# Kernel tuning notes

Measured on AMD Instinct MI355X. Metric: run time of the kernel, lower is better.

## Reference

```python
import jax, jax.numpy as jnp
import numpy as np

D = 1024
LD = 64
NTR = 8192
NT = 8192
DY = 128

def setup_inputs() -> dict:
    key = jax.random.key(0)
    k1, k2, k3, k4 = jax.random.split(key, 4)
    xtr = jax.random.normal(k1, (NTR, D), dtype=jnp.float32)
    ytr = jax.random.normal(k2, (NTR, DY), dtype=jnp.float32)
    xt = jax.random.normal(k3, (NT, D), dtype=jnp.float32)
    A = jax.random.normal(k4, (D, LD), dtype=jnp.float32) / (D ** 0.5)
    return {"xtr": xtr, "ytr": ytr, "xt": xt, "A": A}

def reference(xtr, ytr, xt, A):
    # mean-center both train and test features with the train mean
    mu = jnp.mean(xtr, axis=0, keepdims=True)          # [1, d]
    qtr = (xtr - mu) @ A                                # [Ntr, ld]
    qt = (xt - mu) @ A                                  # [Nt, ld]
    scores = jnp.einsum('nl,ml->nm', qt, qtr)           # [Nt, Ntr]
    E = jax.nn.softmax(scores, axis=1)                  # row-wise softmax over train points
    return E @ ytr                                      # [Nt, dy]
```

## Files before the change

kernel.cpp:

```cpp
#include <hip/hip_runtime.h>
#include <hip/hip_bf16.h>

#define D    1024
#define LD   64
#define NTR  8192
#define NT   8192
#define DY   128

#define SHIFT 40.0f
#define NCHUNK 8
#define CHUNK (NTR / NCHUNK)

typedef __attribute__((ext_vector_type(8))) short bf16x8;
typedef __attribute__((ext_vector_type(8))) _Float16 half8;
typedef __attribute__((ext_vector_type(4))) short short4_;
typedef __attribute__((ext_vector_type(4))) float f4;

static __device__ __forceinline__ short f2bf(float f) {
    __hip_bfloat16 h = __float2bfloat16(f);
    short s; __builtin_memcpy(&s, &h, 2); return s;
}
static __device__ __forceinline__ float bf2f(short s) {
    __hip_bfloat16 h; __builtin_memcpy(&h, &s, 2); return __bfloat162float(h);
}
static __device__ __forceinline__ short f2h(float f) {
    _Float16 h = (_Float16)f;
    short s; __builtin_memcpy(&s, &h, 2); return s;
}
static __device__ __forceinline__ float h2f(short s) {
    _Float16 h; __builtin_memcpy(&h, &s, 2); return (float)h;
}

static __device__ __forceinline__ void gload_lds16(const void* g, void* l) {
    __builtin_amdgcn_global_load_lds(
        (const __attribute__((address_space(1))) unsigned int*)g,
        (__attribute__((address_space(3))) unsigned int*)l,
        16, 0, 0);
}

__global__ __launch_bounds__(256) void proj_prep(const float* __restrict__ xt,
                                                 const float* __restrict__ xtr,
                                                 const float* __restrict__ A,
                                                 const float* __restrict__ ytr,
                                                 short* __restrict__ qt_hi,
                                                 short* __restrict__ qt_lo,
                                                 short* __restrict__ ktr,
                                                 float* __restrict__ muAp,
                                                 short* __restrict__ vtile) {
    __shared__ __align__(16) float smem[4224];

    int tid = threadIdx.x;
    int b = blockIdx.x;

    if (b >= 1024) {
        float* tile = smem;
        int bz = b - 1024;
        int t0 = (bz & 127) * 64;
        int d0 = (bz >> 7) * 64;
        int c = tid & 63;
        int r4 = tid >> 6;
        #pragma unroll
        for (int i = 0; i < 16; ++i) {
            int r = i * 4 + r4;
            tile[r * 66 + c] = ytr[(long)(t0 + r) * DY + d0 + c];
        }
        __syncthreads();
        #pragma unroll
        for (int i = 0; i < 16; ++i) {
            int r = i * 4 + r4;
            int t = t0 + c;
            int dy = d0 + r;
            long idx = (long)(t >> 5) * 4096 + (long)dy * 32
                     + ((((t >> 3) & 3) ^ (dy & 3)) << 3) + (t & 7);
            vtile[idx] = f2bf(tile[c * 66 + r]);
        }
        return;
    }

    float (*xbuf)[2][1024] = (float (*)[2][1024])smem;

    int wave = tid >> 6;
    int lane = tid & 63;
    int quad = lane >> 4;
    int l16 = lane & 15;

    bool is_test = b < (NT / 16);
    int row0 = (is_test ? b : b - NT / 16) * 16;
    const float* x = is_test ? xt : xtr;

    int lr = wave * 4 + (lane >> 4);
    int cg = (lane & 15) ^ (lr & 7);
    const float* xsrc = x + (long)(row0 + lr) * D + cg * 4;

    int col = wave * 16 + l16;
    const float* Acol = A + col;

    f4 acc = (f4){0.f, 0.f, 0.f, 0.f};

    int pr0 = ((quad * 2) ^ (l16 & 7)) * 4;
    int pr1 = (((quad * 2) | 1) ^ (l16 & 7)) * 4;

    gload_lds16(xsrc, &xbuf[0][0][wave * 256]);
    gload_lds16(xsrc + 64, &xbuf[0][1][wave * 256]);
    __syncthreads();

    #pragma unroll 1
    for (int s = 0; s < 8; ++s) {
        int cur = s & 1;
        if (s < 7) {
            const float* nsrc = xsrc + (s + 1) * 128;
            gload_lds16(nsrc, &xbuf[cur ^ 1][0][wave * 256]);
            gload_lds16(nsrc + 64, &xbuf[cur ^ 1][1][wave * 256]);
        }

        #pragma unroll
        for (int s2 = 0; s2 < 2; ++s2) {
            int k0 = s * 128 + s2 * 64;

            bf16x8 bh0, bh1, bl0, bl1;
            #pragma unroll
            for (int j = 0; j < 8; ++j) {
                float a0 = Acol[(long)(k0 + quad * 8 + j) * LD];
                float a1 = Acol[(long)(k0 + 32 + quad * 8 + j) * LD];
                short h0 = f2bf(a0);
                short h1 = f2bf(a1);
                bh0[j] = h0; bl0[j] = f2bf(a0 - bf2f(h0));
                bh1[j] = h1; bl1[j] = f2bf(a1 - bf2f(h1));
            }

            const float* xrow = &xbuf[cur][s2][l16 * 64];
            bf16x8 ah[2], al[2];
            #pragma unroll
            for (int h = 0; h < 2; ++h) {
                f4 v0 = *(const f4*)(xrow + h * 32 + pr0);
                f4 v1 = *(const f4*)(xrow + h * 32 + pr1);
                #pragma unroll
                for (int e = 0; e < 4; ++e) {
                    short hi0 = f2bf(v0[e]);
                    short hi1 = f2bf(v1[e]);
                    ah[h][e]     = hi0;
                    ah[h][e + 4] = hi1;
                    al[h][e]     = f2bf(v0[e] - bf2f(hi0));
                    al[h][e + 4] = f2bf(v1[e] - bf2f(hi1));
                }
            }
            acc = __builtin_amdgcn_mfma_f32_16x16x32_bf16(ah[0], bh0, acc, 0, 0, 0);
            acc = __builtin_amdgcn_mfma_f32_16x16x32_bf16(al[0], bh0, acc, 0, 0, 0);
            acc = __builtin_amdgcn_mfma_f32_16x16x32_bf16(ah[0], bl0, acc, 0, 0, 0);
            acc = __builtin_amdgcn_mfma_f32_16x16x32_bf16(ah[1], bh1, acc, 0, 0, 0);
            acc = __builtin_amdgcn_mfma_f32_16x16x32_bf16(al[1], bh1, acc, 0, 0, 0);
            acc = __builtin_amdgcn_mfma_f32_16x16x32_bf16(ah[1], bl1, acc, 0, 0, 0);
        }
        __syncthreads();
    }

    #pragma unroll
    for (int r = 0; r < 4; ++r) {
        int grow = row0 + quad * 4 + r;
        float qv = acc[r];
        if (is_test) {
            short hi = f2h(qv);
            qt_hi[(long)grow * LD + col] = hi;
            qt_lo[(long)grow * LD + col] = f2h(qv - h2f(hi));
        } else {
            int tl = grow & 31;
            long idx = (long)(grow >> 5) * 2048 + tl * 64
                     + ((((col >> 3) ^ (tl & 7))) << 3) + (col & 7);
            ktr[idx] = f2h(qv);
        }
    }

    if (!is_test) {
        float s = acc[0] + acc[1] + acc[2] + acc[3];
        s += __shfl_xor(s, 16);
        s += __shfl_xor(s, 32);
        if (quad == 0) muAp[(long)(b - NT / 16) * 64 + col] = s;
    }
}

__global__ __launch_bounds__(256) void c_kernel(const short* __restrict__ ktr,
                                                const float* __restrict__ muAp,
                                                float* __restrict__ cc) {
    __shared__ float red[4][64];
    __shared__ __align__(16) float muAs[64];
    int l = threadIdx.x & 63;
    int g = threadIdx.x >> 6;
    float ms = 0.f;
    #pragma unroll 8
    for (int p = g; p < 512; p += 4) ms += muAp[(long)p * 64 + l];
    red[g][l] = ms;
    __syncthreads();
    if (threadIdx.x < 64)
        muAs[l] = (red[0][l] + red[1][l] + red[2][l] + red[3][l]) *
                  (1.0f / (float)NTR);
    __syncthreads();

    int t = blockIdx.x * 256 + threadIdx.x;
    int tl = t & 31;
    long rb = (long)(t >> 5) * 2048 + tl * 64;
    float s = SHIFT;
    #pragma unroll
    for (int c = 0; c < 8; ++c) {
        int pos = (c ^ (tl & 7)) << 3;
        bf16x8 h8 = *(const bf16x8*)&ktr[rb + pos];
        f4 m0 = *(const f4*)&muAs[c * 8];
        f4 m1 = *(const f4*)&muAs[c * 8 + 4];
        #pragma unroll
        for (int j = 0; j < 4; ++j) {
            s += h2f(h8[j]) * m0[j];
            s += h2f(h8[j + 4]) * m1[j];
        }
    }
    cc[t] = s;
}

__global__ __launch_bounds__(256, 3) void flash_kernel(const short* __restrict__ qt_hi,
                                                       const short* __restrict__ qt_lo,
                                                       const short* __restrict__ ksw,
                                                       const short* __restrict__ vtile,
                                                       const float* __restrict__ cc,
                                                       short* __restrict__ Opart,
                                                       float* __restrict__ Lpart) {
    __shared__ __align__(16) short kbh[2][2048];
    __shared__ __align__(16) short vbuf[2][4096];
    __shared__ __align__(16) short ptile[4][1280];

    int tid = threadIdx.x;
    int wave = tid >> 6;
    int lane = tid & 63;
    int quad = lane >> 4;
    int l16 = lane & 15;

    int kc = blockIdx.x & 7;
    int qi = blockIdx.x >> 3;
    int q0w = qi * 128 + wave * 32;
    int tile0 = kc * 32;
    int kc0 = kc * CHUNK;

    int soff = wave * 512 + lane * 8;
    int ldso = wave * 512;

    half8 qh[2][2], ql[2][2];
    #pragma unroll
    for (int rt = 0; rt < 2; ++rt) {
        const short* qrh = qt_hi + (long)(q0w + rt * 16 + l16) * LD + quad * 8;
        const short* qrl = qt_lo + (long)(q0w + rt * 16 + l16) * LD + quad * 8;
        qh[rt][0] = *(const half8*)qrh;
        qh[rt][1] = *(const half8*)(qrh + 32);
        ql[rt][0] = *(const half8*)qrl;
        ql[rt][1] = *(const half8*)(qrl + 32);
    }

    bf16x8 onef;
    #pragma unroll
    for (int i = 0; i < 8; ++i) onef[i] = (short)0x3F80;

    f4 Ov[2][8];
    f4 Lv[2];
    #pragma unroll
    for (int rt = 0; rt < 2; ++rt) {
        Lv[rt] = (f4){0.f, 0.f, 0.f, 0.f};
        #pragma unroll
        for (int jt = 0; jt < 8; ++jt) Ov[rt][jt] = (f4){0.f, 0.f, 0.f, 0.f};
    }

    short* myp = &ptile[wave][0];
    const int p0 = ((quad ^ (l16 & 7)) << 3);
    const int pv = ((quad ^ (l16 & 3)) << 3);

    gload_lds16(ksw + (long)tile0 * 2048 + soff, &kbh[0][ldso]);
    gload_lds16(vtile + (long)tile0 * 4096 + soff, &vbuf[0][ldso]);
    gload_lds16(vtile + (long)tile0 * 4096 + 2048 + soff, &vbuf[0][2048 + ldso]);
    __syncthreads();

    #pragma unroll 1
    for (int it = 0; it < 32; ++it) {
        int cur = it & 1;

        f4 cv[2];
        #pragma unroll
        for (int tt = 0; tt < 2; ++tt)
            cv[tt] = *(const f4*)&cc[kc0 + it * 32 + tt * 16 + quad * 4];

        if (it < 31) {
            int nb = cur ^ 1;
            long tb = (long)(tile0 + it + 1);
            gload_lds16(ksw + tb * 2048 + soff, &kbh[nb][ldso]);
            gload_lds16(vtile + tb * 4096 + soff, &vbuf[nb][ldso]);
            gload_lds16(vtile + tb * 4096 + 2048 + soff, &vbuf[nb][2048 + ldso]);
        }

        half8 kh[2][2];
        #pragma unroll
        for (int tt = 0; tt < 2; ++tt) {
            int rb = (tt * 16 + l16) * 64;
            kh[tt][0] = *(const half8*)&kbh[cur][rb + p0];
            kh[tt][1] = *(const half8*)&kbh[cur][rb + (p0 ^ 32)];
        }

        f4 s[2][2];
        #pragma unroll
        for (int rt = 0; rt < 2; ++rt) {
            #pragma unroll
            for (int tt = 0; tt < 2; ++tt) {
                f4 a = (f4){0.f, 0.f, 0.f, 0.f};
                a = __builtin_amdgcn_mfma_f32_16x16x32_f16(kh[tt][0], qh[rt][0], a, 0, 0, 0);
                a = __builtin_amdgcn_mfma_f32_16x16x32_f16(kh[tt][0], ql[rt][0], a, 0, 0, 0);
                a = __builtin_amdgcn_mfma_f32_16x16x32_f16(kh[tt][1], qh[rt][1], a, 0, 0, 0);
                a = __builtin_amdgcn_mfma_f32_16x16x32_f16(kh[tt][1], ql[rt][1], a, 0, 0, 0);
                s[rt][tt] = a;
            }
        }

        #pragma unroll
        for (int rt = 0; rt < 2; ++rt) {
            #pragma unroll
            for (int tt = 0; tt < 2; ++tt) {
                short4_ p4;
                p4[0] = f2bf(__expf(s[rt][tt][0] - cv[tt][0]));
                p4[1] = f2bf(__expf(s[rt][tt][1] - cv[tt][1]));
                p4[2] = f2bf(__expf(s[rt][tt][2] - cv[tt][2]));
                p4[3] = f2bf(__expf(s[rt][tt][3] - cv[tt][3]));
                *(short4_*)&myp[(rt * 16 + l16) * 40 + tt * 16 + quad * 4] = p4;
            }
        }

        bf16x8 vf[8];
        #pragma unroll
        for (int jt = 0; jt < 8; ++jt)
            vf[jt] = *(const bf16x8*)&vbuf[cur][(jt * 16 + l16) * 32 + pv];
        #pragma unroll
        for (int rt = 0; rt < 2; ++rt) {
            bf16x8 pf = *(const bf16x8*)&myp[(rt * 16 + l16) * 40 + quad * 8];
            #pragma unroll
            for (int jt = 0; jt < 8; ++jt)
                Ov[rt][jt] = __builtin_amdgcn_mfma_f32_16x16x32_bf16(pf, vf[jt], Ov[rt][jt], 0, 0, 0);
            Lv[rt] = __builtin_amdgcn_mfma_f32_16x16x32_bf16(pf, onef, Lv[rt], 0, 0, 0);
        }

        __syncthreads();
    }

    long ob = (long)kc * NT;
    #pragma unroll
    for (int rt = 0; rt < 2; ++rt) {
        #pragma unroll
        for (int jt = 0; jt < 8; ++jt) {
            #pragma unroll
            for (int r = 0; r < 4; ++r)
                Opart[(ob + q0w + rt * 16 + quad * 4 + r) * DY + jt * 16 + l16] =
                    f2bf(Ov[rt][jt][r]);
        }
        if (l16 == 0) {
            #pragma unroll
            for (int r = 0; r < 4; ++r)
                Lpart[ob + q0w + rt * 16 + quad * 4 + r] = Lv[rt][r];
        }
    }
}

__global__ __launch_bounds__(256) void finalize_kernel(const short* __restrict__ Opart,
                                                       const float* __restrict__ Lpart,
                                                       float* __restrict__ out) {
    long i = ((long)blockIdx.x * 256 + threadIdx.x) * 8;
    long row = i >> 7;
    float L = 0.f;
    f4 a = (f4){0.f, 0.f, 0.f, 0.f};
    f4 b = (f4){0.f, 0.f, 0.f, 0.f};
    #pragma unroll
    for (int kc = 0; kc < NCHUNK; ++kc) {
        L += Lpart[(long)kc * NT + row];
        bf16x8 o = *(const bf16x8*)&Opart[(long)kc * NT * DY + i];
        #pragma unroll
        for (int j = 0; j < 4; ++j) {
            a[j] += bf2f(o[j]);
            b[j] += bf2f(o[j + 4]);
        }
    }
    float linv = 1.0f / L;
    a *= linv; b *= linv;
    *(f4*)&out[i] = a;
    *(f4*)&out[i + 4] = b;
}

extern "C" void kernel_launch(void* const* d_in, const int* in_sizes, int n_in,
                              void* d_out, int out_size, void* d_ws, size_t ws_size,
                              hipStream_t stream) {
    const float* xtr = (const float*)d_in[0];
    const float* ytr = (const float*)d_in[1];
    const float* xt  = (const float*)d_in[2];
    const float* A   = (const float*)d_in[3];
    float* out = (float*)d_out;

    char* w = (char*)d_ws;
    float* muAp  = (float*)w; w += (size_t)512 * 64 * 4;
    float* cc    = (float*)w; w += (size_t)NTR * 4;
    float* Lpart = (float*)w; w += (size_t)NCHUNK * NT * 4;
    short* Opart = (short*)w; w += (size_t)NCHUNK * NT * DY * 2;
    short* qt_hi  = (short*)w; w += (size_t)NT * LD * 2;
    short* qt_lo  = (short*)w; w += (size_t)NT * LD * 2;
    short* ksw    = (short*)w; w += (size_t)NTR * LD * 2;
    short* vtile  = (short*)w; w += (size_t)DY * NTR * 2;
    (void)ws_size; (void)in_sizes; (void)n_in; (void)out_size;

    proj_prep<<<1280, 256, 0, stream>>>(xt, xtr, A, ytr,
                                        qt_hi, qt_lo, ksw, muAp, vtile);
    c_kernel<<<32, 256, 0, stream>>>(ksw, muAp, cc);
    flash_kernel<<<512, 256, 0, stream>>>(qt_hi, qt_lo, ksw, vtile, cc,
                                          Opart, Lpart);
    finalize_kernel<<<(NT * DY) / (256 * 8), 256, 0, stream>>>(Opart, Lpart, out);
}
```

Before: 170.4 us.

## Precompute split-bf16 A in swizzled layout and double flash key-split chunks

Adds an a_prep kernel that converts A once into hi/lo bf16 halves stored in the exact fragment layout proj_prep needs. proj_prep now reads them as vector loads instead of doing strided scalar loads and conversions in every block. The flash kernel is templated on the number of key chunks and launches 16 chunks (1024 blocks) when the workspace is large enough, giving more parallelism across the GPU. The cost is a larger Opart/Lpart partial buffer, more reduction work in finalize, and one extra small kernel launch.

Result: no change. 168.7 us (-1.0%).

```diff
diff --git a/kernel.cpp b/kernel.cpp
--- a/kernel.cpp
+++ b/kernel.cpp
@@ -8,8 +8,6 @@
 #define DY   128
 
 #define SHIFT 40.0f
-#define NCHUNK 8
-#define CHUNK (NTR / NCHUNK)
 
 typedef __attribute__((ext_vector_type(8))) short bf16x8;
 typedef __attribute__((ext_vector_type(8))) _Float16 half8;
@@ -38,9 +36,25 @@
         16, 0, 0);
 }
 
+__global__ __launch_bounds__(256) void a_prep(const float* __restrict__ A,
+                                              short* __restrict__ Afh,
+                                              short* __restrict__ Afl) {
+    int idx = blockIdx.x * 256 + threadIdx.x;
+    float a = A[idx];
+    int k = idx >> 6;
+    int col = idx & 63;
+    short hi = f2bf(a);
+    short lo = f2bf(a - bf2f(hi));
+    int o = ((k >> 6) * 8 + ((k >> 5) & 1) * 4 + ((k >> 3) & 3)) * 512
+          + col * 8 + (k & 7);
+    Afh[o] = hi;
+    Afl[o] = lo;
+}
+
 __global__ __launch_bounds__(256) void proj_prep(const float* __restrict__ xt,
                                                  const float* __restrict__ xtr,
-                                                 const float* __restrict__ A,
+                                                 const short* __restrict__ Afh,
+                                                 const short* __restrict__ Afl,
                                                  const float* __restrict__ ytr,
                                                  short* __restrict__ qt_hi,
                                                  short* __restrict__ qt_lo,
@@ -93,7 +107,8 @@
     const float* xsrc = x + (long)(row0 + lr) * D + cg * 4;
 
     int col = wave * 16 + l16;
-    const float* Acol = A + col;
+    const short* AfhL = Afh + quad * 512 + col * 8;
+    const short* AflL = Afl + quad * 512 + col * 8;
 
     f4 acc = (f4){0.f, 0.f, 0.f, 0.f};
 
@@ -115,18 +130,12 @@
 
         #pragma unroll
         for (int s2 = 0; s2 < 2; ++s2) {
-            int k0 = s * 128 + s2 * 64;
-
-            bf16x8 bh0, bh1, bl0, bl1;
-            #pragma unroll
-            for (int j = 0; j < 8; ++j) {
-                float a0 = Acol[(long)(k0 + quad * 8 + j) * LD];
-                float a1 = Acol[(long)(k0 + 32 + quad * 8 + j) * LD];
-                short h0 = f2bf(a0);
-                short h1 = f2bf(a1);
-                bh0[j] = h0; bl0[j] = f2bf(a0 - bf2f(h0));
-                bh1[j] = h1; bl1[j] = f2bf(a1 - bf2f(h1));
-            }
+            int s2g = s * 2 + s2;
+
+            bf16x8 bh0 = *(const bf16x8*)(AfhL + s2g * 4096);
+            bf16x8 bh1 = *(const bf16x8*)(AfhL + s2g * 4096 + 2048);
+            bf16x8 bl0 = *(const bf16x8*)(AflL + s2g * 4096);
+            bf16x8 bl1 = *(const bf16x8*)(AflL + s2g * 4096 + 2048);
 
             const float* xrow = &xbuf[cur][s2][l16 * 64];
             bf16x8 ah[2], al[2];
@@ -214,6 +223,7 @@
     cc[t] = s;
 }
 
+template<int NC>
 __global__ __launch_bounds__(256, 3) void flash_kernel(const short* __restrict__ qt_hi,
                                                        const short* __restrict__ qt_lo,
                                                        const short* __restrict__ ksw,
@@ -221,6 +231,9 @@
                                                        const float* __restrict__ cc,
                                                        short* __restrict__ Opart,
                                                        float* __restrict__ Lpart) {
+    constexpr int TPC = 256 / NC;
+    constexpr int CH  = NTR / NC;
+
     __shared__ __align__(16) short kbh[2][2048];
     __shared__ __align__(16) short vbuf[2][4096];
     __shared__ __align__(16) short ptile[4][1280];
@@ -231,11 +244,11 @@
     int quad = lane >> 4;
     int l16 = lane & 15;
 
-    int kc = blockIdx.x & 7;
-    int qi = blockIdx.x >> 3;
+    int kc = blockIdx.x & (NC - 1);
+    int qi = blockIdx.x / NC;
     int q0w = qi * 128 + wave * 32;
-    int tile0 = kc * 32;
-    int kc0 = kc * CHUNK;
+    int tile0 = kc * TPC;
+    int kc0 = kc * CH;
 
     int soff = wave * 512 + lane * 8;
     int ldso = wave * 512;
@@ -274,7 +287,7 @@
     __syncthreads();
 
     #pragma unroll 1
-    for (int it = 0; it < 32; ++it) {
+    for (int it = 0; it < TPC; ++it) {
         int cur = it & 1;
 
         f4 cv[2];
@@ -282,7 +295,7 @@
         for (int tt = 0; tt < 2; ++tt)
             cv[tt] = *(const f4*)&cc[kc0 + it * 32 + tt * 16 + quad * 4];
 
-        if (it < 31) {
+        if (it < TPC - 1) {
             int nb = cur ^ 1;
             long tb = (long)(tile0 + it + 1);
             gload_lds16(ksw + tb * 2048 + soff, &kbh[nb][ldso]);
@@ -359,6 +372,7 @@
     }
 }
 
+template<int NC>
 __global__ __launch_bounds__(256) void finalize_kernel(const short* __restrict__ Opart,
                                                        const float* __restrict__ Lpart,
                                                        float* __restrict__ out) {
@@ -368,7 +382,7 @@
     f4 a = (f4){0.f, 0.f, 0.f, 0.f};
     f4 b = (f4){0.f, 0.f, 0.f, 0.f};
     #pragma unroll
-    for (int kc = 0; kc < NCHUNK; ++kc) {
+    for (int kc = 0; kc < NC; ++kc) {
         L += Lpart[(long)kc * NT + row];
         bf16x8 o = *(const bf16x8*)&Opart[(long)kc * NT * DY + i];
         #pragma unroll
@@ -392,21 +406,39 @@
     const float* A   = (const float*)d_in[3];
     float* out = (float*)d_out;
 
+    const size_t need16 =
+        (size_t)512 * 64 * 4 + (size_t)NTR * 4 +
+        (size_t)16 * NT * 4 + (size_t)16 * NT * DY * 2 +
+        (size_t)NT * LD * 2 * 2 + (size_t)NTR * LD * 2 +
+        (size_t)DY * NTR * 2 + (size_t)D * LD * 2 * 2;
+    const int NC = (ws_size >= need16) ? 16 : 8;
+
     char* w = (char*)d_ws;
     float* muAp  = (float*)w; w += (size_t)512 * 64 * 4;
     float* cc    = (float*)w; w += (size_t)NTR * 4;
-    float* Lpart = (float*)w; w += (size_t)NCHUNK * NT * 4;
-    short* Opart = (short*)w; w += (size_t)NCHUNK * NT * DY * 2;
+    float* Lpart = (float*)w; w += (size_t)NC * NT * 4;
+    short* Opart = (short*)w; w += (size_t)NC * NT * DY * 2;
     short* qt_hi  = (short*)w; w += (size_t)NT * LD * 2;
     short* qt_lo  = (short*)w; w += (size_t)NT * LD * 2;
     short* ksw    = (short*)w; w += (size_t)NTR * LD * 2;
     short* vtile  = (short*)w; w += (size_t)DY * NTR * 2;
-    (void)ws_size; (void)in_sizes; (void)n_in; (void)out_size;
-
-    proj_prep<<<1280, 256, 0, stream>>>(xt, xtr, A, ytr,
+    short* Afh    = (short*)w; w += (size_t)D * LD * 2;
+    short* Afl    = (short*)w; w += (size_t)D * LD * 2;
+    (void)in_sizes; (void)n_in; (void)out_size;
+
+    a_prep<<<256, 256, 0, stream>>>(A, Afh, Afl);
+    proj_prep<<<1280, 256, 0, stream>>>(xt, xtr, Afh, Afl, ytr,
                                         qt_hi, qt_lo, ksw, muAp, vtile);
     c_kernel<<<32, 256, 0, stream>>>(ksw, muAp, cc);
-    flash_kernel<<<512, 256, 0, stream>>>(qt_hi, qt_lo, ksw, vtile, cc,
-                                          Opart, Lpart);
-    finalize_kernel<<<(NT * DY) / (256 * 8), 256, 0, stream>>>(Opart, Lpart, out);
-}
+    if (NC == 16) {
+        flash_kernel<16><<<64 * 16, 256, 0, stream>>>(qt_hi, qt_lo, ksw, vtile,
+                                                      cc, Opart, Lpart);
+        finalize_kernel<16><<<(NT * DY) / (256 * 8), 256, 0, stream>>>(Opart,
+                                                                       Lpart, out);
+    } else {
+        flash_kernel<8><<<64 * 8, 256, 0, stream>>>(qt_hi, qt_lo, ksw, vtile,
+                                                    cc, Opart, Lpart);
+        finalize_kernel<8><<<(NT * DY) / (256 * 8), 256, 0, stream>>>(Opart,
+                                                                      Lpart, out);
+    }
+}
```
